# Kernel tuning notes

Hardware: AMD Instinct MI355X
Metric: run time of the kernel (lower is better)

Reference implementation:

```python
import jax, jax.numpy as jnp
import numpy as np

BS, NQ, D = 4, 12500, 256
HEADS, LEVELS, POINTS = 8, 2, 4
HD = D // HEADS
D_FF = 2048
SHAPES = ((100, 100), (50, 50))   # (H, W) per level; sum(H*W) == NQ
STARTS = (0, 10000)


def layer_norm(x, g, b, eps=1e-5):
    m = x.mean(-1, keepdims=True)
    v = ((x - m) ** 2).mean(-1, keepdims=True)
    return (x - m) * jax.lax.rsqrt(v + eps) * g + b


def bilinear_sample(value_l, loc, H, W):
    # value_l: (bs, heads, H*W, hd); loc: (bs, heads, nq, P, 2) normalized [0,1]
    # matches F.grid_sample(align_corners=False, padding_mode='zeros')
    x = loc[..., 0] * W - 0.5
    y = loc[..., 1] * H - 0.5
    x0 = jnp.floor(x)
    y0 = jnp.floor(y)
    wx1 = x - x0
    wy1 = y - y0
    wx0 = 1.0 - wx1
    wy0 = 1.0 - wy1
    x0i = x0.astype(jnp.int32)
    y0i = y0.astype(jnp.int32)

    def gather(xi, yi):
        valid = (xi >= 0) & (xi < W) & (yi >= 0) & (yi < H)
        idx = jnp.clip(yi, 0, H - 1) * W + jnp.clip(xi, 0, W - 1)  # (bs,heads,nq,P)
        b, h, nq, P = idx.shape
        g = jnp.take_along_axis(value_l, idx.reshape(b, h, nq * P, 1), axis=2)
        g = g.reshape(b, h, nq, P, -1)
        return g * valid[..., None].astype(g.dtype)

    g00 = gather(x0i, y0i)
    g10 = gather(x0i + 1, y0i)
    g01 = gather(x0i, y0i + 1)
    g11 = gather(x0i + 1, y0i + 1)
    return (g00 * (wx0 * wy0)[..., None] + g10 * (wx1 * wy0)[..., None]
            + g01 * (wx0 * wy1)[..., None] + g11 * (wx1 * wy1)[..., None])


def setup_inputs() -> dict:
    key = jax.random.key(0)
    ks = jax.random.split(key, 20)
    s = 0.02
    inp = {
        'query': jax.random.normal(ks[0], (BS, NQ, D), jnp.float32),
        'reference_points': jax.random.uniform(ks[1], (BS, NQ, LEVELS, 2), jnp.float32),
        'w_off': s * jax.random.normal(ks[2], (D, HEADS * LEVELS * POINTS * 2), jnp.float32),
        'b_off': s * jax.random.normal(ks[3], (HEADS * LEVELS * POINTS * 2,), jnp.float32),
        'w_attn': s * jax.random.normal(ks[4], (D, HEADS * LEVELS * POINTS), jnp.float32),
        'b_attn': s * jax.random.normal(ks[5], (HEADS * LEVELS * POINTS,), jnp.float32),
        'w_val': s * jax.random.normal(ks[6], (D, D), jnp.float32),
        'b_val': jnp.zeros((D,), jnp.float32),
        'w_out': s * jax.random.normal(ks[7], (D, D), jnp.float32),
        'b_out': jnp.zeros((D,), jnp.float32),
        'w1': s * jax.random.normal(ks[8], (D, D_FF), jnp.float32),
        'b1': jnp.zeros((D_FF,), jnp.float32),
        'w2': s * jax.random.normal(ks[9], (D_FF, D), jnp.float32),
        'b2': jnp.zeros((D,), jnp.float32),
        'ln0_g': jnp.ones((D,), jnp.float32),
        'ln0_b': jnp.zeros((D,), jnp.float32),
        'ln1_g': jnp.ones((D,), jnp.float32),
        'ln1_b': jnp.zeros((D,), jnp.float32),
    }
    return inp


def reference(query, reference_points, w_off, b_off, w_attn, b_attn, w_val, b_val,
              w_out, b_out, w1, b1, w2, b2, ln0_g, ln0_b, ln1_g, ln1_b):
    bs, nq, _ = query.shape
    # value projection; encoder self-attention: value == query tokens
    value = (query @ w_val + b_val).reshape(bs, nq, HEADS, HD).transpose(0, 2, 1, 3)  # (bs,heads,nv,hd)
    off = (query @ w_off + b_off).reshape(bs, nq, HEADS, LEVELS, POINTS, 2)
    aw = (query @ w_attn + b_attn).reshape(bs, nq, HEADS, LEVELS * POINTS)
    aw = jax.nn.softmax(aw, axis=-1).reshape(bs, nq, HEADS, LEVELS, POINTS)

    out = jnp.zeros((bs, HEADS, nq, HD), query.dtype)
    for l, (H, W) in enumerate(SHAPES):
        normalizer = jnp.array([W, H], query.dtype)
        # (bs,nq,heads,P,2)
        loc = reference_points[:, :, None, l, None, :] + off[:, :, :, l] / normalizer
        loc = loc.transpose(0, 2, 1, 3, 4)  # (bs,heads,nq,P,2)
        v_l = value[:, :, STARTS[l]:STARTS[l] + H * W]  # (bs,heads,H*W,hd)
        sampled = bilinear_sample(v_l, loc, H, W)       # (bs,heads,nq,P,hd)
        w_l = aw[:, :, :, l].transpose(0, 2, 1, 3)      # (bs,heads,nq,P)
        out = out + (sampled * w_l[..., None]).sum(axis=3)

    attn_out = out.transpose(0, 2, 1, 3).reshape(bs, nq, D) @ w_out + b_out
    x = layer_norm(query + attn_out, ln0_g, ln0_b)
    h = jax.nn.relu(x @ w1 + b1)
    x = layer_norm(x + (h @ w2 + b2), ln1_g, ln1_b)
    return x
```

## Files before the change

kernel.cpp:

```cpp
#include <hip/hip_runtime.h>


#define NQv 12500
#define BSv 4
#define Dv  256
#define DFF 2048

typedef __attribute__((ext_vector_type(8))) __bf16 bf16x8;
typedef __attribute__((ext_vector_type(4))) float f32x4;

__device__ __forceinline__ ushort f32_to_bf16(float f) {
  unsigned u = __float_as_uint(f);
  u += 0x7FFFu + ((u >> 16) & 1u);
  return (ushort)(u >> 16);
}
__device__ __forceinline__ float bf16_to_f32(ushort u) {
  return __uint_as_float(((unsigned)u) << 16);
}

__global__ __launch_bounds__(256) void conv_bf16_kernel(
    const float* __restrict__ in, ushort* __restrict__ out, int n4) {
  int i = blockIdx.x * 256 + threadIdx.x;
  if (i >= n4) return;
  float4 v = reinterpret_cast<const float4*>(in)[i];
  uint2 st;
  st.x = (unsigned)f32_to_bf16(v.x) | ((unsigned)f32_to_bf16(v.y) << 16);
  st.y = (unsigned)f32_to_bf16(v.z) | ((unsigned)f32_to_bf16(v.w) << 16);
  reinterpret_cast<uint2*>(out)[i] = st;
}

__global__ __launch_bounds__(256) void ttrans_kernel(
    const float* __restrict__ in, ushort* __restrict__ out, int K, int N) {
  __shared__ ushort tl[64][65];
  const int n0 = blockIdx.x * 64, k0 = blockIdx.y * 64;
  const int t = threadIdx.x;
#pragma unroll
  for (int i = 0; i < 16; ++i) {
    int idx = t + 256 * i;
    int r = idx >> 6, c = idx & 63;
    tl[r][c] = f32_to_bf16(in[(size_t)(k0 + r) * N + n0 + c]);
  }
  __syncthreads();
#pragma unroll
  for (int i = 0; i < 16; ++i) {
    int idx = t + 256 * i;
    int r = idx >> 6, c = idx & 63;
    out[(size_t)(n0 + r) * K + k0 + c] = tl[c][r];
  }
}

__global__ __launch_bounds__(256) void build_wcat_kernel(
    const float* __restrict__ w_val, const float* __restrict__ w_off,
    const float* __restrict__ w_attn, const float* __restrict__ b_val,
    const float* __restrict__ b_off, const float* __restrict__ b_attn,
    ushort* __restrict__ wcat, float* __restrict__ bcat) {
  int i = blockIdx.x * 256 + threadIdx.x;
  if (i < 448 * 256) {
    int n = i >> 8, k = i & 255;
    float v = (n < 256) ? w_val[(size_t)k * 256 + n]
              : (n < 384) ? w_off[(size_t)k * 128 + (n - 256)]
                          : w_attn[(size_t)k * 64 + (n - 384)];
    wcat[i] = f32_to_bf16(v);
  }
  if (i < 512)
    bcat[i] = (i < 256) ? b_val[i] : (i < 384) ? b_off[i - 256]
              : (i < 448) ? b_attn[i - 384] : 0.f;
}

#define TBM 128
#define TBN 128
#define TBK 32

template <int RELU, int NMASK>
__global__ __launch_bounds__(256) void gemm128_kernel(
    const ushort* __restrict__ A, const ushort* __restrict__ Bt,
    const float* __restrict__ bias, ushort* __restrict__ C,
    int M, int K, int ldc, int Nreal) {
  __shared__ ushort lds[4][TBM * TBK];

  const int t = threadIdx.x;
  const int wid = t >> 6, lane = t & 63;
  const int wr = wid >> 1, wc = wid & 1;
  const int m0 = blockIdx.y * TBM;
  const int n0 = blockIdx.x * TBN;

  int srowA[2], srowB[2], gsl[2];
#pragma unroll
  for (int i = 0; i < 2; i++) {
    int row = i * 64 + (t >> 2);
    int ar = m0 + row;
    srowA[i] = (ar < M) ? ar : (M - 1);
    srowB[i] = n0 + row;
    gsl[i] = ((t & 3) ^ ((row >> 1) & 3)) * 8;
  }

  f32x4 acc[4][4] = {};
  const int nt = K / TBK;
  int cur = 0;

#pragma unroll
  for (int i = 0; i < 2; i++) {
    const int ldsoff = (i * 256 + wid * 64) * 8;
    __builtin_amdgcn_global_load_lds(
        (const __attribute__((address_space(1))) void*)(A + (size_t)srowA[i] * K + gsl[i]),
        (__attribute__((address_space(3))) void*)(lds[0] + ldsoff), 16, 0, 0);
    __builtin_amdgcn_global_load_lds(
        (const __attribute__((address_space(1))) void*)(Bt + (size_t)srowB[i] * K + gsl[i]),
        (__attribute__((address_space(3))) void*)(lds[1] + ldsoff), 16, 0, 0);
  }
  __syncthreads();

  const int rl = lane & 15, kh = lane >> 4;
  for (int tk = 0; tk < nt; ++tk) {
    if (tk + 1 < nt) {
      const int k0 = (tk + 1) * TBK;
      const int nb = (cur ^ 1) * 2;
#pragma unroll
      for (int i = 0; i < 2; i++) {
        const int ldsoff = (i * 256 + wid * 64) * 8;
        __builtin_amdgcn_global_load_lds(
            (const __attribute__((address_space(1))) void*)(A + (size_t)srowA[i] * K + k0 + gsl[i]),
            (__attribute__((address_space(3))) void*)(lds[nb] + ldsoff), 16, 0, 0);
        __builtin_amdgcn_global_load_lds(
            (const __attribute__((address_space(1))) void*)(Bt + (size_t)srowB[i] * K + k0 + gsl[i]),
            (__attribute__((address_space(3))) void*)(lds[nb + 1] + ldsoff), 16, 0, 0);
      }
    }
    {
      const ushort* As = lds[cur * 2];
      const ushort* Bs = lds[cur * 2 + 1];
      bf16x8 afr[4], bfr[4];
#pragma unroll
      for (int ni = 0; ni < 4; ni++) {
        int rowb = wc * 64 + ni * 16 + rl;
        int p = kh ^ ((rowb >> 1) & 3);
        bfr[ni] = *reinterpret_cast<const bf16x8*>(Bs + rowb * 32 + p * 8);
      }
#pragma unroll
      for (int mi = 0; mi < 4; mi++) {
        int rowa = wr * 64 + mi * 16 + rl;
        int p = kh ^ ((rowa >> 1) & 3);
        afr[mi] = *reinterpret_cast<const bf16x8*>(As + rowa * 32 + p * 8);
      }
#pragma unroll
      for (int mi = 0; mi < 4; mi++)
#pragma unroll
        for (int ni = 0; ni < 4; ni++)
          acc[mi][ni] = __builtin_amdgcn_mfma_f32_16x16x32_bf16(afr[mi], bfr[ni], acc[mi][ni], 0, 0, 0);
    }
    __syncthreads();
    cur ^= 1;
  }

  ushort* ldsC = lds[0];
  const int rgrp = lane >> 4, cl = lane & 15;
#pragma unroll
  for (int pass = 0; pass < 2; ++pass) {
    if (wr == pass) {
#pragma unroll
      for (int mi = 0; mi < 4; mi++) {
#pragma unroll
        for (int ni = 0; ni < 4; ni++) {
          int col = wc * 64 + ni * 16 + cl;
          float bv = bias[n0 + col];
#pragma unroll
          for (int r = 0; r < 4; r++) {
            int rloc = mi * 16 + rgrp * 4 + r;
            float v = acc[mi][ni][r] + bv;
            if (RELU) v = fmaxf(v, 0.f);
            ldsC[rloc * 132 + col] = f32_to_bf16(v);
          }
        }
      }
    }
    __syncthreads();
    {
      int rloc = t >> 2;
      int row = m0 + pass * 64 + rloc;
      if (row < M) {
#pragma unroll
        for (int j = 0; j < 4; j++) {
          int col = (t & 3) * 32 + j * 8;
          if (!NMASK || n0 + col < Nreal) {
            uint4 v = *reinterpret_cast<const uint4*>(ldsC + rloc * 132 + col);
            *reinterpret_cast<uint4*>(C + (size_t)row * ldc + n0 + col) = v;
          }
        }
      }
    }
    __syncthreads();
  }
}

__global__ __launch_bounds__(512, 1) void ffn_ln_fused_kernel(
    const ushort* __restrict__ xb,
    const ushort* __restrict__ w1t,
    const float* __restrict__ b1,
    const ushort* __restrict__ w2t,
    const float* __restrict__ b2,
    const float* __restrict__ g1, const float* __restrict__ be1,
    float* __restrict__ out,
    int M) {
  __shared__ ushort lds_all[74752];
  ushort* As = lds_all;
  ushort* Hs = lds_all + 32768;
  ushort* stg0 = lds_all + 50176;

  const int t = threadIdx.x;
  const int wv = t >> 6;
  const int wm = wv >> 2;
  const int wn = wv & 3;
  const int lane = t & 63;
  const int rl = lane & 15, kq = lane >> 4;
  const int cl = lane & 15, g4 = lane >> 4;
  const int m0 = blockIdx.x * 128;

  const int b1row = t >> 3, b1slot = t & 7;
  const int b2row = t >> 2, b2slot = t & 3;

  auto stg = [&](int i) { return stg0 + i * 8192; };

  auto issueB1 = [&](int p, int j, ushort* dst) {
#pragma unroll
    for (int ii = 0; ii < 2; ++ii) {
      int row = b1row + 64 * ii;
      int g = b1slot ^ (row & 7);
      __builtin_amdgcn_global_load_lds(
          (const __attribute__((address_space(1))) void*)(
              w1t + (size_t)(p * 128 + row) * 256 + j * 64 + g * 8),
          (__attribute__((address_space(3))) void*)(dst + (t + 512 * ii) * 8), 16, 0, 0);
    }
  };
  auto issueB2 = [&](int p, int tt, ushort* dst) {
#pragma unroll
    for (int ii = 0; ii < 2; ++ii) {
      int row = b2row + 128 * ii;
      int g = b2slot ^ ((row >> 1) & 3);
      __builtin_amdgcn_global_load_lds(
          (const __attribute__((address_space(1))) void*)(
              w2t + (size_t)row * 2048 + p * 128 + tt * 32 + g * 8),
          (__attribute__((address_space(3))) void*)(dst + (t + 512 * ii) * 8), 16, 0, 0);
    }
  };

#pragma unroll
  for (int ii = 0; ii < 8; ++ii) {
    int row = (t >> 5) + 16 * ii;
    int g = (t & 31) ^ (row & 7);
    int ar = m0 + row; ar = (ar < M) ? ar : (M - 1);
    __builtin_amdgcn_global_load_lds(
        (const __attribute__((address_space(1))) void*)(xb + (size_t)ar * 256 + g * 8),
        (__attribute__((address_space(3))) void*)(As + (t + 512 * ii) * 8), 16, 0, 0);
  }
  issueB1(0, 0, stg(0));
  issueB1(0, 1, stg(1));
  asm volatile("s_waitcnt vmcnt(2)" ::: "memory");
  __builtin_amdgcn_s_barrier();

  f32x4 acc1[4][2] = {};
  f32x4 accF[4][4] = {};
  int cur = 0;

  for (int p = 0; p < 16; ++p) {
#pragma unroll
    for (int j = 0; j < 8; ++j) {
      int tgt = cur + 2; if (tgt >= 3) tgt -= 3;
      if (!(p == 15 && j >= 6)) {
        const int j2 = (j + 2) & 7;
        const int p2 = p + ((j + 2) >> 3);
        if (j2 < 4) issueB1(p2, j2, stg(tgt));
        else issueB2(p2, j2 - 4, stg(tgt));
      }

      const ushort* Bs = stg(cur);
      bf16x8 a1[4][2], b1f[2][2];
      bf16x8 a2[4], b2f[4];
      if (j < 4) {
#pragma unroll
        for (int kk = 0; kk < 2; ++kk) {
          const int slotA = j * 8 + kk * 4 + kq;
#pragma unroll
          for (int mi = 0; mi < 4; mi++) {
            int rowa = wm * 64 + mi * 16 + rl;
            a1[mi][kk] = *reinterpret_cast<const bf16x8*>(As + rowa * 256 + (slotA ^ (rowa & 7)) * 8);
          }
          const int slotB = kk * 4 + kq;
#pragma unroll
          for (int ni = 0; ni < 2; ni++) {
            int rowb = wn * 32 + ni * 16 + rl;
            b1f[ni][kk] = *reinterpret_cast<const bf16x8*>(Bs + rowb * 64 + (slotB ^ (rowb & 7)) * 8);
          }
        }
      } else {
        const int tt = j - 4;
#pragma unroll
        for (int mi = 0; mi < 4; mi++) {
          int rowa = wm * 64 + mi * 16 + rl;
          a2[mi] = *reinterpret_cast<const bf16x8*>(Hs + rowa * 136 + (tt * 4 + kq) * 8);
        }
#pragma unroll
        for (int ni = 0; ni < 4; ni++) {
          int rowb = wn * 64 + ni * 16 + rl;
          b2f[ni] = *reinterpret_cast<const bf16x8*>(Bs + rowb * 32 + (kq ^ ((rowb >> 1) & 3)) * 8);
        }
      }

      __builtin_amdgcn_s_barrier();
      asm volatile("s_waitcnt lgkmcnt(0)" ::: "memory");
      __builtin_amdgcn_sched_barrier(0);

      __builtin_amdgcn_s_setprio(1);
      if (j < 4) {
#pragma unroll
        for (int kk = 0; kk < 2; ++kk)
#pragma unroll
          for (int mi = 0; mi < 4; mi++)
#pragma unroll
            for (int ni = 0; ni < 2; ni++)
              acc1[mi][ni] = __builtin_amdgcn_mfma_f32_16x16x32_bf16(a1[mi][kk], b1f[ni][kk], acc1[mi][ni], 0, 0, 0);
      } else {
#pragma unroll
        for (int mi = 0; mi < 4; mi++)
#pragma unroll
          for (int ni = 0; ni < 4; ni++)
            accF[mi][ni] = __builtin_amdgcn_mfma_f32_16x16x32_bf16(a2[mi], b2f[ni], accF[mi][ni], 0, 0, 0);
      }
      __builtin_amdgcn_s_setprio(0);

      if (j == 3) {
#pragma unroll
        for (int ni = 0; ni < 2; ni++) {
          int col = wn * 32 + ni * 16 + cl;
          float b1v = b1[p * 128 + col];
#pragma unroll
          for (int mi = 0; mi < 4; mi++) {
#pragma unroll
            for (int r = 0; r < 4; r++) {
              int row = wm * 64 + mi * 16 + g4 * 4 + r;
              Hs[row * 136 + col] = f32_to_bf16(fmaxf(acc1[mi][ni][r] + b1v, 0.f));
            }
          }
        }
#pragma unroll
        for (int mi = 0; mi < 4; mi++)
#pragma unroll
          for (int ni = 0; ni < 2; ni++)
            acc1[mi][ni] = (f32x4){0.f, 0.f, 0.f, 0.f};
      }

      if (!(p == 15 && j >= 6)) {
        asm volatile("s_waitcnt vmcnt(2) lgkmcnt(0)" ::: "memory");
      } else if (j == 6) {
        asm volatile("s_waitcnt vmcnt(0) lgkmcnt(0)" ::: "memory");
      } else {
        asm volatile("s_waitcnt lgkmcnt(0)" ::: "memory");
      }
      __builtin_amdgcn_s_barrier();
      cur = cur + 1; if (cur >= 3) cur -= 3;
    }
  }

  float* ptab = (float*)stg0;
  float* mtab = (float*)(stg0 + 2048);

  float b2c[4], g1c[4], bec[4];
#pragma unroll
  for (int ni = 0; ni < 4; ni++) {
    int col = wn * 64 + ni * 16 + cl;
    b2c[ni] = b2[col]; g1c[ni] = g1[col]; bec[ni] = be1[col];
  }
#pragma unroll
  for (int mi = 0; mi < 4; mi++) {
#pragma unroll
    for (int ni = 0; ni < 4; ni++) {
      int col = wn * 64 + ni * 16 + cl;
#pragma unroll
      for (int r = 0; r < 4; r++) {
        int row = wm * 64 + mi * 16 + g4 * 4 + r;
        ushort xv = As[row * 256 + ((col >> 3) ^ (row & 7)) * 8 + (col & 7)];
        accF[mi][ni][r] += b2c[ni] + bf16_to_f32(xv);
      }
    }
  }
#pragma unroll
  for (int mi = 0; mi < 4; mi++) {
#pragma unroll
    for (int r = 0; r < 4; r++) {
      float s = accF[mi][0][r] + accF[mi][1][r] + accF[mi][2][r] + accF[mi][3][r];
      float sq = accF[mi][0][r] * accF[mi][0][r] + accF[mi][1][r] * accF[mi][1][r] +
                 accF[mi][2][r] * accF[mi][2][r] + accF[mi][3][r] * accF[mi][3][r];
#pragma unroll
      for (int o = 1; o < 16; o <<= 1) {
        s += __shfl_xor(s, o, 64);
        sq += __shfl_xor(sq, o, 64);
      }
      if (cl == 0) {
        int row = wm * 64 + mi * 16 + g4 * 4 + r;
        ptab[(row * 4 + wn) * 2 + 0] = s;
        ptab[(row * 4 + wn) * 2 + 1] = sq;
      }
    }
  }
  __syncthreads();
  {
    int row = t >> 2, part = t & 3;
    float s = ptab[(row * 4 + part) * 2 + 0];
    float sq = ptab[(row * 4 + part) * 2 + 1];
    s += __shfl_xor(s, 1, 64);  sq += __shfl_xor(sq, 1, 64);
    s += __shfl_xor(s, 2, 64);  sq += __shfl_xor(sq, 2, 64);
    if (part == 0) {
      float mean = s * (1.f / 256.f);
      float var = sq * (1.f / 256.f) - mean * mean;
      mtab[row * 2 + 0] = mean;
      mtab[row * 2 + 1] = rsqrtf(var + 1e-5f);
    }
  }
  __syncthreads();
#pragma unroll
  for (int mi = 0; mi < 4; mi++) {
#pragma unroll
    for (int r = 0; r < 4; r++) {
      int row = wm * 64 + mi * 16 + g4 * 4 + r;
      float2 ms = *reinterpret_cast<const float2*>(mtab + row * 2);
      int grow = m0 + row;
      if (grow < M) {
#pragma unroll
        for (int ni = 0; ni < 4; ni++) {
          int col = wn * 64 + ni * 16 + cl;
          out[(size_t)grow * 256 + col] = (accF[mi][ni][r] - ms.x) * ms.y * g1c[ni] + bec[ni];
        }
      }
    }
  }
}

__global__ __launch_bounds__(256) void deform_attn_kernel(
    const ushort* __restrict__ pcat, const float* __restrict__ refp,
    ushort* __restrict__ out, int total) {
  int tid = blockIdx.x * 256 + threadIdx.x;
  if (tid >= total) return;
  int c0 = (tid & 3) * 8;
  int idx = tid >> 2;
  int h = idx & 7;
  int row = idx >> 3;
  int bl = row / NQv;

  const ushort* prow = pcat + (size_t)row * 448;

  ushort awr[8];
  *reinterpret_cast<uint4*>(awr) = *reinterpret_cast<const uint4*>(prow + 384 + h * 8);
  float lg[8], mx = -1e30f;
#pragma unroll
  for (int i = 0; i < 8; i++) { lg[i] = bf16_to_f32(awr[i]); mx = fmaxf(mx, lg[i]); }
  float ssum = 0.f;
#pragma unroll
  for (int i = 0; i < 8; i++) { lg[i] = __expf(lg[i] - mx); ssum += lg[i]; }
  float inv = 1.f / ssum;

  ushort ofr[16];
  *reinterpret_cast<uint4*>(ofr)     = *reinterpret_cast<const uint4*>(prow + 256 + h * 16);
  *reinterpret_cast<uint4*>(ofr + 8) = *reinterpret_cast<const uint4*>(prow + 256 + h * 16 + 8);
  float4 rp = *reinterpret_cast<const float4*>(refp + (size_t)row * 4);

  float acc8[8] = {};
  const int Ws[2] = {100, 50}, Hs2[2] = {100, 50}, Ss[2] = {0, 10000};
#pragma unroll
  for (int l = 0; l < 2; l++) {
    const int W = Ws[l], H = Hs2[l];
    float fx = (l ? rp.z : rp.x) * (float)W - 0.5f;
    float fy = (l ? rp.w : rp.y) * (float)H - 0.5f;
    const ushort* vbase = pcat + ((size_t)bl * NQv + Ss[l]) * 448 + h * 32 + c0;
#pragma unroll
    for (int p = 0; p < 4; p++) {
      float x = fx + bf16_to_f32(ofr[l * 8 + p * 2 + 0]);
      float y = fy + bf16_to_f32(ofr[l * 8 + p * 2 + 1]);
      float x0f = floorf(x), y0f = floorf(y);
      float wx1 = x - x0f, wy1 = y - y0f;
      float wx0 = 1.f - wx1, wy0 = 1.f - wy1;
      int x0 = (int)x0f, y0 = (int)y0f;
      float aw = lg[l * 4 + p] * inv;

      float cw[4] = {aw * wx0 * wy0, aw * wx1 * wy0, aw * wx0 * wy1, aw * wx1 * wy1};
      int cx[4] = {x0, x0 + 1, x0, x0 + 1};
      int cy[4] = {y0, y0, y0 + 1, y0 + 1};
#pragma unroll
      for (int c = 0; c < 4; c++) {
        int xi = cx[c], yi = cy[c];
        if (xi >= 0 && xi < W && yi >= 0 && yi < H) {
          ushort vr[8];
          *reinterpret_cast<uint4*>(vr) =
              *reinterpret_cast<const uint4*>(vbase + (size_t)(yi * W + xi) * 448);
          float w = cw[c];
#pragma unroll
          for (int j = 0; j < 8; j++) acc8[j] += w * bf16_to_f32(vr[j]);
        }
      }
    }
  }

  ushort st[8];
#pragma unroll
  for (int j = 0; j < 8; j++) st[j] = f32_to_bf16(acc8[j]);
  *reinterpret_cast<uint4*>(out + (size_t)row * 256 + h * 32 + c0) =
      *reinterpret_cast<uint4*>(st);
}

__global__ __launch_bounds__(256) void ln0_kernel(
    const float* __restrict__ A, const ushort* __restrict__ B,
    const float* __restrict__ gamma, const float* __restrict__ beta,
    ushort* __restrict__ outb, int M) {
  int row = blockIdx.x * 4 + (threadIdx.x >> 6);
  int lane = threadIdx.x & 63;
  if (row >= M) return;
  size_t base = (size_t)row * 256 + lane * 4;
  float4 a = *reinterpret_cast<const float4*>(A + base);
  uint2 braw = *reinterpret_cast<const uint2*>(B + base);
  float x0 = a.x + bf16_to_f32((ushort)(braw.x & 0xffffu));
  float x1 = a.y + bf16_to_f32((ushort)(braw.x >> 16));
  float x2 = a.z + bf16_to_f32((ushort)(braw.y & 0xffffu));
  float x3 = a.w + bf16_to_f32((ushort)(braw.y >> 16));
  float s = x0 + x1 + x2 + x3;
  float sq = x0 * x0 + x1 * x1 + x2 * x2 + x3 * x3;
#pragma unroll
  for (int o = 1; o < 64; o <<= 1) {
    s += __shfl_xor(s, o, 64);
    sq += __shfl_xor(sq, o, 64);
  }
  float mean = s * (1.f / 256.f);
  float var = sq * (1.f / 256.f) - mean * mean;
  float rs = rsqrtf(var + 1e-5f);
  float4 gv = *reinterpret_cast<const float4*>(gamma + lane * 4);
  float4 bv = *reinterpret_cast<const float4*>(beta + lane * 4);
  float o0 = (x0 - mean) * rs * gv.x + bv.x;
  float o1 = (x1 - mean) * rs * gv.y + bv.y;
  float o2 = (x2 - mean) * rs * gv.z + bv.z;
  float o3 = (x3 - mean) * rs * gv.w + bv.w;
  uint2 st;
  st.x = (unsigned)f32_to_bf16(o0) | ((unsigned)f32_to_bf16(o1) << 16);
  st.y = (unsigned)f32_to_bf16(o2) | ((unsigned)f32_to_bf16(o3) << 16);
  *reinterpret_cast<uint2*>(outb + base) = st;
}

extern "C" void kernel_launch(void* const* d_in, const int* in_sizes, int n_in,
                              void* d_out, int out_size, void* d_ws, size_t ws_size,
                              hipStream_t stream) {
  const float* query  = (const float*)d_in[0];
  const float* refp   = (const float*)d_in[1];
  const float* w_off  = (const float*)d_in[2];
  const float* b_off  = (const float*)d_in[3];
  const float* w_attn = (const float*)d_in[4];
  const float* b_attn = (const float*)d_in[5];
  const float* w_val  = (const float*)d_in[6];
  const float* b_val  = (const float*)d_in[7];
  const float* w_out  = (const float*)d_in[8];
  const float* b_out  = (const float*)d_in[9];
  const float* w1     = (const float*)d_in[10];
  const float* b1     = (const float*)d_in[11];
  const float* w2     = (const float*)d_in[12];
  const float* b2     = (const float*)d_in[13];
  const float* ln0g   = (const float*)d_in[14];
  const float* ln0b   = (const float*)d_in[15];
  const float* ln1g   = (const float*)d_in[16];
  const float* ln1b   = (const float*)d_in[17];
  float* outp = (float*)d_out;

  char* ws = (char*)d_ws;
  size_t woff = 0;
  auto walloc = [&](size_t bytes) { size_t r = woff; woff += (bytes + 255) & ~(size_t)255; return r; };
  ushort* wcat = (ushort*)(ws + walloc((size_t)512 * 256 * 2));
  float*  bcat = (float*)(ws + walloc(512 * 4));
  ushort* wqt  = (ushort*)(ws + walloc((size_t)256 * 256 * 2));
  ushort* w1t  = (ushort*)(ws + walloc((size_t)DFF * 256 * 2));
  ushort* w2t  = (ushort*)(ws + walloc((size_t)256 * DFF * 2));
  char* arena = ws + woff;
  size_t arena_sz = (ws_size > woff) ? (ws_size - woff) : 0;

  int nb = ((size_t)BSv * NQv * 1920 + (1u << 20) <= arena_sz) ? BSv : 1;
  const int R = nb * NQv;
  ushort* qb   = (ushort*)arena;
  ushort* pcat = (ushort*)(arena + (size_t)R * 512);
  ushort* samp = (ushort*)(arena + (size_t)R * 1408);
  ushort* proj = qb;
  ushort* xb   = samp;

  build_wcat_kernel<<<dim3(448), dim3(256), 0, stream>>>(
      w_val, w_off, w_attn, b_val, b_off, b_attn, wcat, bcat);
  ttrans_kernel<<<dim3(4, 4), dim3(256), 0, stream>>>(w_out, wqt, Dv, Dv);
  ttrans_kernel<<<dim3(DFF / 64, 4), dim3(256), 0, stream>>>(w1, w1t, Dv, DFF);
  ttrans_kernel<<<dim3(4, DFF / 64), dim3(256), 0, stream>>>(w2, w2t, DFF, Dv);

  const int MT = (R + TBM - 1) / TBM;

  for (int c = 0; c < BSv / nb; c++) {
    const int row0 = c * R;
    const float* qrow = query + (size_t)row0 * Dv;

    conv_bf16_kernel<<<dim3((R * 64 + 255) / 256), dim3(256), 0, stream>>>(qrow, qb, R * 64);

    gemm128_kernel<0, 1><<<dim3(4, MT), dim3(256), 0, stream>>>(
        qb, wcat, bcat, pcat, R, Dv, 448, 448);

    deform_attn_kernel<<<dim3((R * 32 + 255) / 256), dim3(256), 0, stream>>>(
        pcat, refp + (size_t)row0 * 4, samp, R * 32);

    gemm128_kernel<0, 0><<<dim3(2, MT), dim3(256), 0, stream>>>(
        samp, wqt, b_out, proj, R, Dv, 256, 256);

    ln0_kernel<<<dim3((R + 3) / 4), dim3(256), 0, stream>>>(qrow, proj, ln0g, ln0b, xb, R);

    ffn_ln_fused_kernel<<<dim3((R + 127) / 128), dim3(512), 0, stream>>>(
        xb, w1t, b1, w2t, b2, ln1g, ln1b, outp + (size_t)row0 * 256, R);
  }
}
```

Baseline: 357.8 us.

## Load FFN second-GEMM weights directly into registers, bypassing LDS staging

The W2 tiles in the fused FFN+LayerNorm kernel are now loaded from global memory straight into registers with double-buffered register sets (b2rA/b2rB), instead of being staged through LDS by async global_load_lds. Only the W1 tiles still go through the three-stage LDS ring, and their issue schedule is rebuilt around a per-p stage rotation. The H tile pitch shrinks from 136 to 132, which cuts LDS use and may change bank conflicts. The aim is to remove LDS traffic and barrier pressure for W2, at the cost of more VGPRs and global load latency that is exposed if the prefetch distance is too short.

```diff
diff --git a/kernel.cpp b/kernel.cpp
--- a/kernel.cpp
+++ b/kernel.cpp
@@ -192,6 +192,15 @@
   }
 }
 
+#define LOADB2(pp, tt, dst)                                                     \
+  {                                                                             \
+    _Pragma("unroll") for (int ni = 0; ni < 4; ni++) {                          \
+      int rowb = wn * 64 + ni * 16 + rl;                                        \
+      dst[ni] = *reinterpret_cast<const bf16x8*>(                               \
+          w2t + (size_t)rowb * 2048 + (pp) * 128 + ((tt) * 4 + kq) * 8);        \
+    }                                                                           \
+  }
+
 __global__ __launch_bounds__(512, 1) void ffn_ln_fused_kernel(
     const ushort* __restrict__ xb,
     const ushort* __restrict__ w1t,
@@ -201,10 +210,10 @@
     const float* __restrict__ g1, const float* __restrict__ be1,
     float* __restrict__ out,
     int M) {
-  __shared__ ushort lds_all[74752];
+  __shared__ ushort lds_all[74240];
   ushort* As = lds_all;
   ushort* Hs = lds_all + 32768;
-  ushort* stg0 = lds_all + 50176;
+  ushort* stg0 = lds_all + 49664;
 
   const int t = threadIdx.x;
   const int wv = t >> 6;
@@ -216,29 +225,17 @@
   const int m0 = blockIdx.x * 128;
 
   const int b1row = t >> 3, b1slot = t & 7;
-  const int b2row = t >> 2, b2slot = t & 3;
 
   auto stg = [&](int i) { return stg0 + i * 8192; };
 
-  auto issueB1 = [&](int p, int j, ushort* dst) {
+  auto issueB1 = [&](int p, int s, ushort* dst) {
 #pragma unroll
     for (int ii = 0; ii < 2; ++ii) {
       int row = b1row + 64 * ii;
       int g = b1slot ^ (row & 7);
       __builtin_amdgcn_global_load_lds(
           (const __attribute__((address_space(1))) void*)(
-              w1t + (size_t)(p * 128 + row) * 256 + j * 64 + g * 8),
-          (__attribute__((address_space(3))) void*)(dst + (t + 512 * ii) * 8), 16, 0, 0);
-    }
-  };
-  auto issueB2 = [&](int p, int tt, ushort* dst) {
-#pragma unroll
-    for (int ii = 0; ii < 2; ++ii) {
-      int row = b2row + 128 * ii;
-      int g = b2slot ^ ((row >> 1) & 3);
-      __builtin_amdgcn_global_load_lds(
-          (const __attribute__((address_space(1))) void*)(
-              w2t + (size_t)row * 2048 + p * 128 + tt * 32 + g * 8),
+              w1t + (size_t)(p * 128 + row) * 256 + s * 64 + g * 8),
           (__attribute__((address_space(3))) void*)(dst + (t + 512 * ii) * 8), 16, 0, 0);
     }
   };
@@ -259,30 +256,22 @@
 
   f32x4 acc1[4][2] = {};
   f32x4 accF[4][4] = {};
-  int cur = 0;
+  bf16x8 b2rA[4], b2rB[4];
+  int pm3 = 0;
 
   for (int p = 0; p < 16; ++p) {
 #pragma unroll
     for (int j = 0; j < 8; ++j) {
-      int tgt = cur + 2; if (tgt >= 3) tgt -= 3;
-      if (!(p == 15 && j >= 6)) {
-        const int j2 = (j + 2) & 7;
-        const int p2 = p + ((j + 2) >> 3);
-        if (j2 < 4) issueB1(p2, j2, stg(tgt));
-        else issueB2(p2, j2 - 4, stg(tgt));
-      }
-
-      const ushort* Bs = stg(cur);
-      bf16x8 a1[4][2], b1f[2][2];
-      bf16x8 a2[4], b2f[4];
       if (j < 4) {
+        const ushort* Bs = stg((pm3 + j) % 3);
+        bf16x8 a1f[4][2], b1f[2][2];
 #pragma unroll
         for (int kk = 0; kk < 2; ++kk) {
           const int slotA = j * 8 + kk * 4 + kq;
 #pragma unroll
           for (int mi = 0; mi < 4; mi++) {
             int rowa = wm * 64 + mi * 16 + rl;
-            a1[mi][kk] = *reinterpret_cast<const bf16x8*>(As + rowa * 256 + (slotA ^ (rowa & 7)) * 8);
+            a1f[mi][kk] = *reinterpret_cast<const bf16x8*>(As + rowa * 256 + (slotA ^ (rowa & 7)) * 8);
           }
           const int slotB = kk * 4 + kq;
 #pragma unroll
@@ -291,73 +280,88 @@
             b1f[ni][kk] = *reinterpret_cast<const bf16x8*>(Bs + rowb * 64 + (slotB ^ (rowb & 7)) * 8);
           }
         }
+        if (j == 0) issueB1(p, 2, stg((pm3 + 2) % 3));
+        if (j == 1) issueB1(p, 3, stg(pm3));
+        if (j == 3) LOADB2(p, 0, b2rA);
+
+        asm volatile("s_waitcnt lgkmcnt(0)" ::: "memory");
+        __builtin_amdgcn_sched_barrier(0);
+        __builtin_amdgcn_s_setprio(1);
+#pragma unroll
+        for (int kk = 0; kk < 2; ++kk)
+#pragma unroll
+          for (int mi = 0; mi < 4; mi++)
+#pragma unroll
+            for (int ni = 0; ni < 2; ni++)
+              acc1[mi][ni] = __builtin_amdgcn_mfma_f32_16x16x32_bf16(a1f[mi][kk], b1f[ni][kk], acc1[mi][ni], 0, 0, 0);
+        __builtin_amdgcn_s_setprio(0);
+
+        if (j == 3) {
+#pragma unroll
+          for (int ni = 0; ni < 2; ni++) {
+            int col = wn * 32 + ni * 16 + cl;
+            float b1v = b1[p * 128 + col];
+#pragma unroll
+            for (int mi = 0; mi < 4; mi++) {
+#pragma unroll
+              for (int r = 0; r < 4; r++) {
+                int row = wm * 64 + mi * 16 + g4 * 4 + r;
+                Hs[row * 132 + col] = f32_to_bf16(fmaxf(acc1[mi][ni][r] + b1v, 0.f));
+              }
+            }
+          }
+#pragma unroll
+          for (int mi = 0; mi < 4; mi++)
+#pragma unroll
+            for (int ni = 0; ni < 2; ni++)
+              acc1[mi][ni] = (f32x4){0.f, 0.f, 0.f, 0.f};
+        }
+
+        if (j == 0) asm volatile("s_waitcnt vmcnt(2)" ::: "memory");
+        if (j == 1) asm volatile("s_waitcnt vmcnt(2)" ::: "memory");
+        if (j == 2) asm volatile("s_waitcnt vmcnt(0)" ::: "memory");
+        if (j == 3) asm volatile("s_waitcnt lgkmcnt(0)" ::: "memory");
+        __builtin_amdgcn_s_barrier();
       } else {
         const int tt = j - 4;
+        bf16x8 a2f[4];
 #pragma unroll
         for (int mi = 0; mi < 4; mi++) {
           int rowa = wm * 64 + mi * 16 + rl;
-          a2[mi] = *reinterpret_cast<const bf16x8*>(Hs + rowa * 136 + (tt * 4 + kq) * 8);
-        }
-#pragma unroll
-        for (int ni = 0; ni < 4; ni++) {
-          int rowb = wn * 64 + ni * 16 + rl;
-          b2f[ni] = *reinterpret_cast<const bf16x8*>(Bs + rowb * 32 + (kq ^ ((rowb >> 1) & 3)) * 8);
-        }
-      }
-
-      __builtin_amdgcn_s_barrier();
-      asm volatile("s_waitcnt lgkmcnt(0)" ::: "memory");
-      __builtin_amdgcn_sched_barrier(0);
-
-      __builtin_amdgcn_s_setprio(1);
-      if (j < 4) {
-#pragma unroll
-        for (int kk = 0; kk < 2; ++kk)
+          a2f[mi] = *reinterpret_cast<const bf16x8*>(Hs + rowa * 132 + (tt * 4 + kq) * 8);
+        }
+        if (p < 15) {
+          if (j == 4) issueB1(p + 1, 0, stg((pm3 + 1) % 3));
+          if (j == 5) issueB1(p + 1, 1, stg((pm3 + 2) % 3));
+        }
+        if (j == 4) LOADB2(p, 1, b2rB);
+        if (j == 5) LOADB2(p, 2, b2rA);
+        if (j == 6) LOADB2(p, 3, b2rB);
+
+        asm volatile("s_waitcnt lgkmcnt(0)" ::: "memory");
+        __builtin_amdgcn_sched_barrier(0);
+        __builtin_amdgcn_s_setprio(1);
+        if ((tt & 1) == 0) {
 #pragma unroll
           for (int mi = 0; mi < 4; mi++)
 #pragma unroll
-            for (int ni = 0; ni < 2; ni++)
-              acc1[mi][ni] = __builtin_amdgcn_mfma_f32_16x16x32_bf16(a1[mi][kk], b1f[ni][kk], acc1[mi][ni], 0, 0, 0);
-      } else {
-#pragma unroll
-        for (int mi = 0; mi < 4; mi++)
-#pragma unroll
-          for (int ni = 0; ni < 4; ni++)
-            accF[mi][ni] = __builtin_amdgcn_mfma_f32_16x16x32_bf16(a2[mi], b2f[ni], accF[mi][ni], 0, 0, 0);
-      }
-      __builtin_amdgcn_s_setprio(0);
-
-      if (j == 3) {
-#pragma unroll
-        for (int ni = 0; ni < 2; ni++) {
-          int col = wn * 32 + ni * 16 + cl;
-          float b1v = b1[p * 128 + col];
-#pragma unroll
-          for (int mi = 0; mi < 4; mi++) {
-#pragma unroll
-            for (int r = 0; r < 4; r++) {
-              int row = wm * 64 + mi * 16 + g4 * 4 + r;
-              Hs[row * 136 + col] = f32_to_bf16(fmaxf(acc1[mi][ni][r] + b1v, 0.f));
-            }
-          }
-        }
-#pragma unroll
-        for (int mi = 0; mi < 4; mi++)
-#pragma unroll
-          for (int ni = 0; ni < 2; ni++)
-            acc1[mi][ni] = (f32x4){0.f, 0.f, 0.f, 0.f};
-      }
-
-      if (!(p == 15 && j >= 6)) {
-        asm volatile("s_waitcnt vmcnt(2) lgkmcnt(0)" ::: "memory");
-      } else if (j == 6) {
-        asm volatile("s_waitcnt vmcnt(0) lgkmcnt(0)" ::: "memory");
-      } else {
-        asm volatile("s_waitcnt lgkmcnt(0)" ::: "memory");
-      }
-      __builtin_amdgcn_s_barrier();
-      cur = cur + 1; if (cur >= 3) cur -= 3;
-    }
+            for (int ni = 0; ni < 4; ni++)
+              accF[mi][ni] = __builtin_amdgcn_mfma_f32_16x16x32_bf16(a2f[mi], b2rA[ni], accF[mi][ni], 0, 0, 0);
+        } else {
+#pragma unroll
+          for (int mi = 0; mi < 4; mi++)
+#pragma unroll
+            for (int ni = 0; ni < 4; ni++)
+              accF[mi][ni] = __builtin_amdgcn_mfma_f32_16x16x32_bf16(a2f[mi], b2rB[ni], accF[mi][ni], 0, 0, 0);
+        }
+        __builtin_amdgcn_s_setprio(0);
+
+        if (j == 7 && p < 15)
+          asm volatile("s_waitcnt vmcnt(14)" ::: "memory");
+        __builtin_amdgcn_s_barrier();
+      }
+    }
+    pm3 = pm3 + 1; if (pm3 == 3) pm3 = 0;
   }
 
   float* ptab = (float*)stg0;
```

After: 448.8 us. +25.4%, slower.
